# Performance work log

Hardware: AMD Instinct MI355X
Metric: run time of the kernel (lower is better)

The kernel has to match this reference:

```python
import jax, jax.numpy as jnp
import numpy as np

WS = (7, 7)          # window size
DIM = 256            # projection_dim
HEADS = 8
B = 2048             # batch * num_windows
NW = 64              # windows per image (mask leading dim)


def _relative_position_index(ws):
    coords = np.stack(np.meshgrid(np.arange(ws[0]), np.arange(ws[1]), indexing='ij'))  # [2,h,w]
    flat = coords.reshape(2, -1)                                   # [2, h*w]
    rel = flat[:, :, None] - flat[:, None, :]                      # [2, N, N]
    rel = rel.transpose(1, 2, 0)                                   # [N, N, 2]
    rel[:, :, 0] += ws[0] - 1
    rel[:, :, 1] += ws[1] - 1
    idx = rel[:, :, 0] * (2 * ws[1] - 1) + rel[:, :, 1]            # [N, N]
    return idx.reshape(-1).astype(np.int32)                        # [N*N]


def setup_inputs() -> dict:
    key = jax.random.key(0)
    ks = jax.random.split(key, 6)
    N = WS[0] * WS[1]
    return {
        'x': jax.random.normal(ks[0], (B, N, DIM), jnp.float32),
        'mask': jax.random.normal(ks[1], (NW, N, N), jnp.float32),  # additive shift mask
        'qkv_w': jax.random.normal(ks[2], (DIM, 3 * DIM), jnp.float32) * (DIM ** -0.5),
        'qkv_b': jnp.zeros((3 * DIM,), jnp.float32),
        'proj_w': jax.random.normal(ks[3], (DIM, DIM), jnp.float32) * (DIM ** -0.5),
        'proj_b': jnp.zeros((DIM,), jnp.float32),
        'bias_table': jax.random.normal(ks[4], ((2 * WS[0] - 1) * (2 * WS[1] - 1), HEADS), jnp.float32) * 0.02,
        'rel_index': jnp.asarray(_relative_position_index(WS)),
    }


def reference(x, mask, qkv_w, qkv_b, proj_w, proj_b, bias_table, rel_index):
    Bn, N, C = x.shape
    hd = C // HEADS
    scale = hd ** -0.5
    qkv = x @ qkv_w + qkv_b                               # [B, N, 3C]
    qkv = qkv.reshape(Bn, N, 3, HEADS, hd).transpose(2, 0, 3, 1, 4)  # [3, B, H, N, hd]
    q, k, v = qkv[0], qkv[1], qkv[2]
    attn = jnp.einsum('bhnd,bhmd->bhnm', q * scale, k)    # [B, H, N, N]
    # gathered relative position bias: [N*N, H] -> [H, N, N]
    bias = bias_table[rel_index].reshape(N, N, HEADS).transpose(2, 0, 1)
    attn = attn + bias[None]
    nW = mask.shape[0]
    attn = attn.reshape(Bn // nW, nW, HEADS, N, N) + mask[None, :, None]
    attn = attn.reshape(Bn, HEADS, N, N)
    attn = jax.nn.softmax(attn, axis=-1)
    out = jnp.einsum('bhnm,bhmd->bhnd', attn, v)          # [B, H, N, hd]
    out = out.transpose(0, 2, 1, 3).reshape(Bn, N, C)
    return out @ proj_w + proj_b
```

## Files before the change

### kernel.cpp

```cpp
#include <hip/hip_runtime.h>


typedef __attribute__((ext_vector_type(8))) short v8s;
typedef __attribute__((ext_vector_type(4))) short v4s;
typedef __attribute__((ext_vector_type(4))) float v4f;

__device__ __forceinline__ unsigned short f2bf(float f) {
    union { float f; unsigned int i; } v; v.f = f;
    unsigned int x = v.i;
    return (unsigned short)((x + 0x7fffu + ((x >> 16) & 1u)) >> 16);
}
__device__ __forceinline__ unsigned int pk2bf(float a, float b) {
    return (unsigned int)f2bf(a) | ((unsigned int)f2bf(b) << 16);
}

#define NW1 196608
#define NW2 65536
#define NB1 768
#define NCB 1605632
#define QSCALE_LOG2E 0.25503487f
#define LOG2E 1.4426950408889634f

__global__ void wattn_preproc(const float* __restrict__ qkv_w,
                              const float* __restrict__ qkv_b,
                              const float* __restrict__ proj_w,
                              const float* __restrict__ bias_table,
                              const float* __restrict__ mask,
                              const int* __restrict__ rel_index,
                              unsigned short* __restrict__ W1f,
                              unsigned short* __restrict__ W2f,
                              float* __restrict__ B1v,
                              float* __restrict__ CBf)
{
    const int idx = blockIdx.x * 256 + threadIdx.x;
    if (idx < NW1) {
        const int j = idx & 7, l = (idx >> 3) & 63, s = (idx >> 9) & 7, T = idx >> 12;
        const int k = s * 32 + (l >> 4) * 8 + j;
        const int n = T * 16 + (l & 15);
        const int hh = n / 96, sub = n % 96;
        const int col = (sub < 32) ? (hh * 32 + sub)
                      : (sub < 64) ? (256 + hh * 32 + (sub - 32))
                                   : (512 + hh * 32 + (sub - 64));
        float v = qkv_w[k * 768 + col];
        if (sub < 32) v *= QSCALE_LOG2E;
        W1f[idx] = f2bf(v);
    } else if (idx < NW1 + NW2) {
        const int t = idx - NW1;
        const int j = t & 7, l = (t >> 3) & 63, s = (t >> 9) & 7, T = t >> 12;
        const int k = s * 32 + (l >> 4) * 8 + j;
        const int n = T * 16 + (l & 15);
        W2f[t] = f2bf(proj_w[k * 256 + n]);
    } else if (idx < NW1 + NW2 + NB1) {
        const int n = idx - NW1 - NW2;
        const int hh = n / 96, sub = n % 96;
        const int col = (sub < 32) ? (hh * 32 + sub)
                      : (sub < 64) ? (256 + hh * 32 + (sub - 32))
                                   : (512 + hh * 32 + (sub - 64));
        float v = qkv_b[col];
        if (sub < 32) v *= QSCALE_LOG2E;
        B1v[n] = v;
    } else {
        const int t = idx - (NW1 + NW2 + NB1);
        if (t < NCB) {
            const int c = t & 63;
            const int rr = t >> 6;
            const int r = rr % 49;
            const int q2 = rr / 49;
            const int hh = q2 & 7;
            const int w = q2 >> 3;
            const int c_old = ((c & 3) << 4) | (c >> 2);
            float v;
            if (c_old < 49) {
                const int ri = rel_index[r * 49 + c_old];
                v = (bias_table[ri * 8 + hh] + mask[(w * 49 + r) * 49 + c_old]) * LOG2E;
            } else {
                v = -1e30f;
            }
            CBf[t] = v;
        }
    }
}

__global__ __launch_bounds__(256, 2)
void wattn_main(const float* __restrict__ x,
                const unsigned short* __restrict__ W1f,
                const float* __restrict__ B1v,
                const float* __restrict__ CB,
                const unsigned short* __restrict__ W2f,
                const float* __restrict__ proj_b,
                float* __restrict__ out)
{
    __shared__ __align__(16) unsigned short wreg[4 * 3528];
    __shared__ __align__(16) unsigned short Os[49 * 264];
    unsigned short* const xs = wreg;

    const int tid  = threadIdx.x;
    const int wave = tid >> 6;
    const int lane = tid & 63;
    const int quad = lane >> 4;
    const int l15  = lane & 15;
    const int b    = blockIdx.x;
    const int widx = b & 63;
    const float* xw = x + (long)b * 49 * 256;
    const v4f zero4 = {0.0f, 0.0f, 0.0f, 0.0f};
    unsigned short* const Wr = wreg + wave * 3528;

    int arow[4];
    #pragma unroll
    for (int mt = 0; mt < 4; ++mt) {
        int m = mt * 16 + l15; if (m > 48) m = 48;
        arow[mt] = m * 136 + quad * 8;
    }

    #pragma unroll 1
    for (int p = 0; p < 2; ++p) {
        v4f acc[6][4];
        #pragma unroll
        for (int i = 0; i < 6; ++i)
            #pragma unroll
            for (int mt = 0; mt < 4; ++mt) acc[i][mt] = zero4;

        const int T0 = p * 24 + wave * 6;
        const unsigned short* bb = W1f + T0 * 4096 + lane * 8;

        #pragma unroll 1
        for (int ch = 0; ch < 2; ++ch) {
            __syncthreads();
            for (int i = tid; i < 1568; i += 256) {
                const int r = i >> 5, cq = i & 31;
                const float4 v = *reinterpret_cast<const float4*>(xw + r * 256 + ch * 128 + cq * 4);
                ushort4 o;
                o.x = f2bf(v.x); o.y = f2bf(v.y); o.z = f2bf(v.z); o.w = f2bf(v.w);
                *reinterpret_cast<ushort4*>(&xs[r * 136 + cq * 4]) = o;
            }
            __syncthreads();
            #pragma unroll 2
            for (int s = 0; s < 4; ++s) {
                v8s afr[4];
                #pragma unroll
                for (int mt = 0; mt < 4; ++mt)
                    afr[mt] = *reinterpret_cast<const v8s*>(&xs[arow[mt] + s * 32]);
                v8s bfr[6];
                #pragma unroll
                for (int i = 0; i < 6; ++i)
                    bfr[i] = *reinterpret_cast<const v8s*>(bb + i * 4096 + (ch * 4 + s) * 512);
                #pragma unroll
                for (int i = 0; i < 6; ++i)
                    #pragma unroll
                    for (int mt = 0; mt < 4; ++mt)
                        acc[i][mt] = __builtin_amdgcn_mfma_f32_16x16x32_bf16(afr[mt], bfr[i], acc[i][mt], 0, 0, 0);
            }
        }
        #pragma unroll
        for (int i = 0; i < 6; ++i) {
            const float bv = B1v[(T0 + i) * 16 + l15];
            #pragma unroll
            for (int mt = 0; mt < 4; ++mt) {
                acc[i][mt].x += bv; acc[i][mt].y += bv; acc[i][mt].z += bv; acc[i][mt].w += bv;
            }
        }

        unsigned int vpk[2][4][2];
        #pragma unroll
        for (int iv = 0; iv < 2; ++iv)
            #pragma unroll
            for (int mt = 0; mt < 4; ++mt) {
                vpk[iv][mt][0] = pk2bf(acc[4 + iv][mt][0], acc[4 + iv][mt][1]);
                vpk[iv][mt][1] = pk2bf(acc[4 + iv][mt][2], acc[4 + iv][mt][3]);
            }

        __syncthreads();

        const int h = p * 4 + wave;

        #pragma unroll
        for (int i = 0; i < 4; ++i) {
            const int base = (i < 2) ? 0 : 1764;
            const int c = (i & 1) * 16 + l15;
            #pragma unroll
            for (int mt = 0; mt < 4; ++mt) {
                const int m0 = mt * 16 + quad * 4;
                #pragma unroll
                for (int r = 0; r < 4; ++r)
                    if (m0 + r < 49) Wr[base + (m0 + r) * 36 + c] = f2bf(acc[i][mt][r]);
            }
        }

        v8s aq[4], bk[4];
        #pragma unroll
        for (int t = 0; t < 4; ++t) {
            int rq = t * 16 + l15; if (rq > 48) rq = 48;
            const int qo = rq * 36 + quad * 8;
            const v4s qlo = *reinterpret_cast<const v4s*>(&Wr[qo]);
            const v4s qhi = *reinterpret_cast<const v4s*>(&Wr[qo + 4]);
            aq[t] = __builtin_shufflevector(qlo, qhi, 0, 1, 2, 3, 4, 5, 6, 7);
            const v4s klo = *reinterpret_cast<const v4s*>(&Wr[1764 + qo]);
            const v4s khi = *reinterpret_cast<const v4s*>(&Wr[1764 + qo + 4]);
            bk[t] = __builtin_shufflevector(klo, khi, 0, 1, 2, 3, 4, 5, 6, 7);
        }

        const float* cbb = CB + ((long)widx * 8 + h) * 49 * 64;
        #pragma unroll 2
        for (int mt = 0; mt < 4; ++mt) {
            v4f sacc[4];
            #pragma unroll
            for (int nt = 0; nt < 4; ++nt)
                sacc[nt] = __builtin_amdgcn_mfma_f32_16x16x32_bf16(aq[mt], bk[nt], zero4, 0, 0, 0);
            #pragma unroll
            for (int r = 0; r < 4; ++r) {
                const int m = mt * 16 + quad * 4 + r;
                const int mc = m > 48 ? 48 : m;
                const float4 cb4 = *reinterpret_cast<const float4*>(cbb + mc * 64 + l15 * 4);
                float s0 = sacc[0][r] + cb4.x;
                float s1 = sacc[1][r] + cb4.y;
                float s2 = sacc[2][r] + cb4.z;
                float s3 = sacc[3][r] + cb4.w;
                float mx = fmaxf(fmaxf(s0, s1), fmaxf(s2, s3));
                #pragma unroll
                for (int off = 1; off < 16; off <<= 1) mx = fmaxf(mx, __shfl_xor(mx, off, 16));
                const float e0 = __builtin_exp2f(s0 - mx);
                const float e1 = __builtin_exp2f(s1 - mx);
                const float e2 = __builtin_exp2f(s2 - mx);
                const float e3 = __builtin_exp2f(s3 - mx);
                float sm = (e0 + e1) + (e2 + e3);
                #pragma unroll
                for (int off = 1; off < 16; off <<= 1) sm += __shfl_xor(sm, off, 16);
                const float rs = __builtin_amdgcn_rcpf(sm);
                if (m < 49) {
                    Wr[m * 72 + l15]      = f2bf(e0 * rs);
                    Wr[m * 72 + 16 + l15] = f2bf(e1 * rs);
                    Wr[m * 72 + 32 + l15] = f2bf(e2 * rs);
                    Wr[m * 72 + 48 + l15] = f2bf(e3 * rs);
                }
            }
        }

        const int srcA = ((quad & 1) << 5) + l15;
        v8s bvf[2][2];
        #pragma unroll
        for (int kt = 0; kt < 2; ++kt) {
            #pragma unroll
            for (int iv = 0; iv < 2; ++iv) {
                union { unsigned int u[4]; v8s v; } bw;
                #pragma unroll
                for (int hw = 0; hw < 2; ++hw) {
                    const unsigned int aA = (unsigned int)__shfl((int)vpk[iv][2 * kt][hw],     srcA);
                    const unsigned int bA = (unsigned int)__shfl((int)vpk[iv][2 * kt + 1][hw], srcA);
                    bw.u[hw] = (quad & 2) ? bA : aA;
                    const unsigned int aB = (unsigned int)__shfl((int)vpk[iv][2 * kt][hw],     srcA + 16);
                    const unsigned int bB = (unsigned int)__shfl((int)vpk[iv][2 * kt + 1][hw], srcA + 16);
                    bw.u[2 + hw] = (quad & 2) ? bB : aB;
                }
                bvf[kt][iv] = bw.v;
            }
        }

        #pragma unroll
        for (int mt = 0; mt < 4; ++mt) {
            int mrc = mt * 16 + l15; if (mrc > 48) mrc = 48;
            v4f oacc[2] = {zero4, zero4};
            #pragma unroll
            for (int kt = 0; kt < 2; ++kt) {
                const v8s ap = *reinterpret_cast<const v8s*>(&Wr[mrc * 72 + kt * 32 + quad * 8]);
                oacc[0] = __builtin_amdgcn_mfma_f32_16x16x32_bf16(ap, bvf[kt][0], oacc[0], 0, 0, 0);
                oacc[1] = __builtin_amdgcn_mfma_f32_16x16x32_bf16(ap, bvf[kt][1], oacc[1], 0, 0, 0);
            }
            #pragma unroll
            for (int n2 = 0; n2 < 2; ++n2) {
                const int c = h * 32 + n2 * 16 + l15;
                #pragma unroll
                for (int r = 0; r < 4; ++r) {
                    const int m = mt * 16 + quad * 4 + r;
                    if (m < 49) Os[m * 264 + c] = f2bf(oacc[n2][r]);
                }
            }
        }
    }

    __syncthreads();

    v4f pacc[4][4];
    #pragma unroll
    for (int i = 0; i < 4; ++i)
        #pragma unroll
        for (int mt = 0; mt < 4; ++mt) pacc[i][mt] = zero4;

    int orow[4];
    #pragma unroll
    for (int mt = 0; mt < 4; ++mt) {
        int m = mt * 16 + l15; if (m > 48) m = 48;
        orow[mt] = m * 264 + quad * 8;
    }
    const unsigned short* wb = W2f + (wave * 4) * 4096 + lane * 8;

    #pragma unroll 2
    for (int s = 0; s < 8; ++s) {
        v8s afr[4];
        #pragma unroll
        for (int mt = 0; mt < 4; ++mt)
            afr[mt] = *reinterpret_cast<const v8s*>(&Os[orow[mt] + s * 32]);
        #pragma unroll
        for (int i = 0; i < 4; ++i) {
            const v8s bfp = *reinterpret_cast<const v8s*>(wb + i * 4096 + s * 512);
            #pragma unroll
            for (int mt = 0; mt < 4; ++mt)
                pacc[i][mt] = __builtin_amdgcn_mfma_f32_16x16x32_bf16(afr[mt], bfp, pacc[i][mt], 0, 0, 0);
        }
    }

    #pragma unroll
    for (int i = 0; i < 4; ++i) {
        const int c = (wave * 4 + i) * 16 + l15;
        const float pb = proj_b[c];
        #pragma unroll
        for (int mt = 0; mt < 4; ++mt) {
            #pragma unroll
            for (int r = 0; r < 4; ++r) {
                const int m = mt * 16 + quad * 4 + r;
                if (m < 49) out[((long)b * 49 + m) * 256 + c] = pacc[i][mt][r] + pb;
            }
        }
    }
}

extern "C" void kernel_launch(void* const* d_in, const int* in_sizes, int n_in,
                              void* d_out, int out_size, void* d_ws, size_t ws_size,
                              hipStream_t stream)
{
    const float* x          = (const float*)d_in[0];
    const float* mask       = (const float*)d_in[1];
    const float* qkv_w      = (const float*)d_in[2];
    const float* qkv_b      = (const float*)d_in[3];
    const float* proj_w     = (const float*)d_in[4];
    const float* proj_b     = (const float*)d_in[5];
    const float* bias_table = (const float*)d_in[6];
    const int*   rel_index  = (const int*)d_in[7];
    float* out = (float*)d_out;

    char* ws = (char*)d_ws;
    unsigned short* W1f = (unsigned short*)(ws);
    unsigned short* W2f = (unsigned short*)(ws + 393216);
    float*          B1v = (float*)(ws + 524288);
    float*          CBf = (float*)(ws + 527360);

    wattn_preproc<<<7299, 256, 0, stream>>>(qkv_w, qkv_b, proj_w, bias_table, mask,
                                            rel_index, W1f, W2f, B1v, CBf);
    wattn_main<<<2048, 256, 0, stream>>>(x, W1f, B1v, CBf, W2f, proj_b, out);
}
```

Measured before the change: 406.9 us.

## Shrink LDS footprint by splitting projection per head-pass and smaller x staging

Reduces shared memory by staging x in 64-column chunks instead of 128, widening the per-wave Q/K scratch stride to allow single 16-byte loads, and performing the output projection per head-pass using only half of the attention output. The first pass writes the partial projection to global output and the second pass read-modify-writes it. This is meant to cut LDS usage so more blocks fit per CU, at the cost of extra global traffic on the output and more barrier/load rounds for x.

```diff
diff --git a/kernel.cpp b/kernel.cpp
--- a/kernel.cpp
+++ b/kernel.cpp
@@ -2,7 +2,6 @@
 
 
 typedef __attribute__((ext_vector_type(8))) short v8s;
-typedef __attribute__((ext_vector_type(4))) short v4s;
 typedef __attribute__((ext_vector_type(4))) float v4f;
 
 __device__ __forceinline__ unsigned short f2bf(float f) {
@@ -90,9 +89,9 @@
                 const float* __restrict__ proj_b,
                 float* __restrict__ out)
 {
-    __shared__ __align__(16) unsigned short wreg[4 * 3528];
-    __shared__ __align__(16) unsigned short Os[49 * 264];
-    unsigned short* const xs = wreg;
+    __shared__ __align__(16) unsigned short xs[49 * 72];
+    __shared__ __align__(16) unsigned short wreg[4 * 3920];
+    unsigned short* const Osp = wreg;
 
     const int tid  = threadIdx.x;
     const int wave = tid >> 6;
@@ -103,13 +102,13 @@
     const int widx = b & 63;
     const float* xw = x + (long)b * 49 * 256;
     const v4f zero4 = {0.0f, 0.0f, 0.0f, 0.0f};
-    unsigned short* const Wr = wreg + wave * 3528;
+    unsigned short* const Wr = wreg + wave * 3920;
 
     int arow[4];
     #pragma unroll
     for (int mt = 0; mt < 4; ++mt) {
         int m = mt * 16 + l15; if (m > 48) m = 48;
-        arow[mt] = m * 136 + quad * 8;
+        arow[mt] = m * 72 + quad * 8;
     }
 
     #pragma unroll 1
@@ -124,18 +123,18 @@
         const unsigned short* bb = W1f + T0 * 4096 + lane * 8;
 
         #pragma unroll 1
-        for (int ch = 0; ch < 2; ++ch) {
+        for (int ch = 0; ch < 4; ++ch) {
             __syncthreads();
-            for (int i = tid; i < 1568; i += 256) {
-                const int r = i >> 5, cq = i & 31;
-                const float4 v = *reinterpret_cast<const float4*>(xw + r * 256 + ch * 128 + cq * 4);
+            for (int i = tid; i < 784; i += 256) {
+                const int r = i >> 4, cq = i & 15;
+                const float4 v = *reinterpret_cast<const float4*>(xw + r * 256 + ch * 64 + cq * 4);
                 ushort4 o;
                 o.x = f2bf(v.x); o.y = f2bf(v.y); o.z = f2bf(v.z); o.w = f2bf(v.w);
-                *reinterpret_cast<ushort4*>(&xs[r * 136 + cq * 4]) = o;
+                *reinterpret_cast<ushort4*>(&xs[r * 72 + cq * 4]) = o;
             }
             __syncthreads();
-            #pragma unroll 2
-            for (int s = 0; s < 4; ++s) {
+            #pragma unroll
+            for (int s = 0; s < 2; ++s) {
                 v8s afr[4];
                 #pragma unroll
                 for (int mt = 0; mt < 4; ++mt)
@@ -143,7 +142,7 @@
                 v8s bfr[6];
                 #pragma unroll
                 for (int i = 0; i < 6; ++i)
-                    bfr[i] = *reinterpret_cast<const v8s*>(bb + i * 4096 + (ch * 4 + s) * 512);
+                    bfr[i] = *reinterpret_cast<const v8s*>(bb + i * 4096 + (ch * 2 + s) * 512);
                 #pragma unroll
                 for (int i = 0; i < 6; ++i)
                     #pragma unroll
@@ -169,20 +168,18 @@
                 vpk[iv][mt][1] = pk2bf(acc[4 + iv][mt][2], acc[4 + iv][mt][3]);
             }
 
-        __syncthreads();
-
         const int h = p * 4 + wave;
 
         #pragma unroll
         for (int i = 0; i < 4; ++i) {
-            const int base = (i < 2) ? 0 : 1764;
+            const int base = (i < 2) ? 0 : 1960;
             const int c = (i & 1) * 16 + l15;
             #pragma unroll
             for (int mt = 0; mt < 4; ++mt) {
                 const int m0 = mt * 16 + quad * 4;
                 #pragma unroll
                 for (int r = 0; r < 4; ++r)
-                    if (m0 + r < 49) Wr[base + (m0 + r) * 36 + c] = f2bf(acc[i][mt][r]);
+                    if (m0 + r < 49) Wr[base + (m0 + r) * 40 + c] = f2bf(acc[i][mt][r]);
             }
         }
 
@@ -190,13 +187,8 @@
         #pragma unroll
         for (int t = 0; t < 4; ++t) {
             int rq = t * 16 + l15; if (rq > 48) rq = 48;
-            const int qo = rq * 36 + quad * 8;
-            const v4s qlo = *reinterpret_cast<const v4s*>(&Wr[qo]);
-            const v4s qhi = *reinterpret_cast<const v4s*>(&Wr[qo + 4]);
-            aq[t] = __builtin_shufflevector(qlo, qhi, 0, 1, 2, 3, 4, 5, 6, 7);
-            const v4s klo = *reinterpret_cast<const v4s*>(&Wr[1764 + qo]);
-            const v4s khi = *reinterpret_cast<const v4s*>(&Wr[1764 + qo + 4]);
-            bk[t] = __builtin_shufflevector(klo, khi, 0, 1, 2, 3, 4, 5, 6, 7);
+            aq[t] = *reinterpret_cast<const v8s*>(&Wr[rq * 40 + quad * 8]);
+            bk[t] = *reinterpret_cast<const v8s*>(&Wr[1960 + rq * 40 + quad * 8]);
         }
 
         const float* cbb = CB + ((long)widx * 8 + h) * 49 * 64;
@@ -255,69 +247,79 @@
             }
         }
 
+        v4f oaccA[4][2];
         #pragma unroll
         for (int mt = 0; mt < 4; ++mt) {
             int mrc = mt * 16 + l15; if (mrc > 48) mrc = 48;
-            v4f oacc[2] = {zero4, zero4};
+            v4f o0 = zero4, o1 = zero4;
             #pragma unroll
             for (int kt = 0; kt < 2; ++kt) {
                 const v8s ap = *reinterpret_cast<const v8s*>(&Wr[mrc * 72 + kt * 32 + quad * 8]);
-                oacc[0] = __builtin_amdgcn_mfma_f32_16x16x32_bf16(ap, bvf[kt][0], oacc[0], 0, 0, 0);
-                oacc[1] = __builtin_amdgcn_mfma_f32_16x16x32_bf16(ap, bvf[kt][1], oacc[1], 0, 0, 0);
-            }
+                o0 = __builtin_amdgcn_mfma_f32_16x16x32_bf16(ap, bvf[kt][0], o0, 0, 0, 0);
+                o1 = __builtin_amdgcn_mfma_f32_16x16x32_bf16(ap, bvf[kt][1], o1, 0, 0, 0);
+            }
+            oaccA[mt][0] = o0; oaccA[mt][1] = o1;
+        }
+
+        __syncthreads();
+        #pragma unroll
+        for (int mt = 0; mt < 4; ++mt) {
             #pragma unroll
             for (int n2 = 0; n2 < 2; ++n2) {
-                const int c = h * 32 + n2 * 16 + l15;
+                const int c = wave * 32 + n2 * 16 + l15;
                 #pragma unroll
                 for (int r = 0; r < 4; ++r) {
                     const int m = mt * 16 + quad * 4 + r;
-                    if (m < 49) Os[m * 264 + c] = f2bf(oacc[n2][r]);
+                    if (m < 49) Osp[m * 136 + c] = f2bf(oaccA[mt][n2][r]);
                 }
             }
         }
-    }
-
-    __syncthreads();
-
-    v4f pacc[4][4];
-    #pragma unroll
-    for (int i = 0; i < 4; ++i)
-        #pragma unroll
-        for (int mt = 0; mt < 4; ++mt) pacc[i][mt] = zero4;
-
-    int orow[4];
-    #pragma unroll
-    for (int mt = 0; mt < 4; ++mt) {
-        int m = mt * 16 + l15; if (m > 48) m = 48;
-        orow[mt] = m * 264 + quad * 8;
-    }
-    const unsigned short* wb = W2f + (wave * 4) * 4096 + lane * 8;
-
-    #pragma unroll 2
-    for (int s = 0; s < 8; ++s) {
-        v8s afr[4];
-        #pragma unroll
-        for (int mt = 0; mt < 4; ++mt)
-            afr[mt] = *reinterpret_cast<const v8s*>(&Os[orow[mt] + s * 32]);
+        __syncthreads();
+
+        v4f pacc[4][4];
+        #pragma unroll
+        for (int i = 0; i < 4; ++i)
+            #pragma unroll
+            for (int mt = 0; mt < 4; ++mt) pacc[i][mt] = zero4;
+
+        int orow[4];
+        #pragma unroll
+        for (int mt = 0; mt < 4; ++mt) {
+            int m = mt * 16 + l15; if (m > 48) m = 48;
+            orow[mt] = m * 136 + quad * 8;
+        }
+        const unsigned short* wb = W2f + (wave * 4) * 4096 + lane * 8;
+
+        #pragma unroll
+        for (int ss = 0; ss < 4; ++ss) {
+            v8s afr[4];
+            #pragma unroll
+            for (int mt = 0; mt < 4; ++mt)
+                afr[mt] = *reinterpret_cast<const v8s*>(&Osp[orow[mt] + ss * 32]);
+            #pragma unroll
+            for (int i = 0; i < 4; ++i) {
+                const v8s bfp = *reinterpret_cast<const v8s*>(wb + i * 4096 + (p * 4 + ss) * 512);
+                #pragma unroll
+                for (int mt = 0; mt < 4; ++mt)
+                    pacc[i][mt] = __builtin_amdgcn_mfma_f32_16x16x32_bf16(afr[mt], bfp, pacc[i][mt], 0, 0, 0);
+            }
+        }
+
         #pragma unroll
         for (int i = 0; i < 4; ++i) {
-            const v8s bfp = *reinterpret_cast<const v8s*>(wb + i * 4096 + s * 512);
-            #pragma unroll
-            for (int mt = 0; mt < 4; ++mt)
-                pacc[i][mt] = __builtin_amdgcn_mfma_f32_16x16x32_bf16(afr[mt], bfp, pacc[i][mt], 0, 0, 0);
-        }
-    }
-
-    #pragma unroll
-    for (int i = 0; i < 4; ++i) {
-        const int c = (wave * 4 + i) * 16 + l15;
-        const float pb = proj_b[c];
-        #pragma unroll
-        for (int mt = 0; mt < 4; ++mt) {
-            #pragma unroll
-            for (int r = 0; r < 4; ++r) {
-                const int m = mt * 16 + quad * 4 + r;
-                if (m < 49) out[((long)b * 49 + m) * 256 + c] = pacc[i][mt][r] + pb;
+            const int c = (wave * 4 + i) * 16 + l15;
+            const float pb = proj_b[c];
+            #pragma unroll
+            for (int mt = 0; mt < 4; ++mt) {
+                #pragma unroll
+                for (int r = 0; r < 4; ++r) {
+                    const int m = mt * 16 + quad * 4 + r;
+                    if (m < 49) {
+                        float* po = &out[((long)b * 49 + m) * 256 + c];
+                        if (p == 0) *po = pacc[i][mt][r] + pb;
+                        else        *po += pacc[i][mt][r];
+                    }
+                }
             }
         }
     }
```

Measured after the change: 521.8 us. 28.2% more time.
